# Optimization experiments

Measured on AMD Instinct MI355X. Metric: run time of the kernel, lower is better.

The kernel has to match this reference:

```python
import jax, jax.numpy as jnp
import numpy as np

N, A, C = 1024, 4096, 10000

def setup_inputs() -> dict:
    key = jax.random.key(0)
    ks = jax.random.split(key, 7)
    features = jax.random.normal(ks[0], (N, A), dtype=jnp.float32)
    labels = jax.random.randint(ks[1], (N,), 0, C, dtype=jnp.int64)
    fc_weight = jax.random.normal(ks[2], (C, A), dtype=jnp.float32) * 0.02
    fc_bias = jax.random.normal(ks[3], (C,), dtype=jnp.float32) * 0.02
    Ave = jax.random.normal(ks[4], (C, A), dtype=jnp.float32)
    CoVariance = jax.random.uniform(ks[5], (C, A), dtype=jnp.float32)
    Amount = jax.random.uniform(ks[6], (C,), dtype=jnp.float32) * 10.0
    return {"features": features, "labels": labels, "fc_weight": fc_weight,
            "fc_bias": fc_bias, "Ave": Ave, "CoVariance": CoVariance,
            "Amount": Amount, "ratio": 1}

def _update_cv(f, labels, Ave, CoVariance, Amount):
    # segment-reduce form of the onehot-masked mean/var in update_CV
    count = jax.ops.segment_sum(jnp.ones((f.shape[0],), f.dtype), labels, num_segments=C)  # [C]
    denom = jnp.maximum(count, 1.0)[:, None]                                               # [C,1]
    ave = jax.ops.segment_sum(f, labels, num_segments=C) / denom                           # [C,A]
    var = jax.ops.segment_sum((f - ave[labels]) ** 2, labels, num_segments=C) / denom      # [C,A]
    tot = count + Amount
    w = (count / jnp.where(tot == 0, 1.0, tot))[:, None]  # weight_CV, NaN->0 handled since count==0 when tot==0
    new_CV = CoVariance * (1.0 - w) + var * w + w * (1.0 - w) * (Ave - ave) ** 2
    new_Ave = Ave * (1.0 - w) + ave * w
    new_Amount = Amount + count
    return new_CV, new_Ave, new_Amount

def reference(features, labels, fc_weight, fc_bias, Ave, CoVariance, Amount, ratio):
    y = features @ fc_weight.T + fc_bias  # [N,C]
    f = jax.lax.stop_gradient(features)
    new_CV, new_Ave, new_Amount = _update_cv(f, labels, Ave, CoVariance, Amount)
    cv = jax.lax.stop_gradient(new_CV)
    # isda_aug: sigma2[n,c] = ratio * sum_a (W[c,a]-W[y_n,a])^2 * CV[y_n,a]
    # expanded into three GEMM/reduction terms to avoid the O(N*C*A) intermediate
    CVn = cv[labels]        # [N,A]
    Wk = fc_weight[labels]  # [N,A]
    term1 = CVn @ (fc_weight ** 2).T                          # [N,C]
    term2 = -2.0 * ((CVn * Wk) @ fc_weight.T)                 # [N,C]
    term3 = jnp.sum(CVn * Wk ** 2, axis=1, keepdims=True)     # [N,1]
    sigma2 = ratio * (term1 + term2 + term3)
    aug = y + 0.5 * sigma2
    logp = jax.nn.log_softmax(aug, axis=-1)
    loss = -jnp.mean(jnp.take_along_axis(logp, labels[:, None], axis=1))
    return (loss, y)
```

## Files before the change

kernel.cpp:

```cpp
#include <hip/hip_runtime.h>
#include <hip/hip_bf16.h>
#include <math.h>

#define NN 1024
#define AA 4096
#define CC 10000
#define NT 79
#define BM 64
#define BN 128

typedef __attribute__((ext_vector_type(8))) short short8;
typedef __attribute__((ext_vector_type(4))) float f32x4;

#define OFF_COUNT   0u
#define OFF_HEAD    40960u
#define OFF_NEXT    81920u
#define OFF_T3H     86016u
#define OFF_RAUG    90112u
#define OFF_PART    94208u
#define OFF_FEATB   741376u
#define OFF_A1B     9129984u
#define OFF_A2B     17518592u
#define WS_BASE     25907200u
#define OFF_WB      25907200u
#define WS_BIG      107827200u

#define A1OFF 8388608u
#define A2OFF 16777216u

__device__ inline unsigned short f2bf(float x) {
    union { float f; unsigned u; } v; v.f = x;
    unsigned r = v.u + 0x7FFFu + ((v.u >> 16) & 1u);
    return (unsigned short)(r >> 16);
}

__device__ __forceinline__ void gload16(const void* g, void* l) {
    __builtin_amdgcn_global_load_lds((const __attribute__((address_space(1))) void*)g,
                                     (__attribute__((address_space(3))) void*)l, 16, 0, 0);
}

__device__ __forceinline__ short8 bfsq(short8 w) {
    union U { short8 s; unsigned u[4]; } in, out;
    in.s = w;
    #pragma unroll
    for (int i = 0; i < 4; i++) {
        unsigned u = in.u[i];
        float lo = __uint_as_float(u << 16);
        float hi = __uint_as_float(u & 0xffff0000u);
        float sl = lo * lo;
        float sh = hi * hi;
        unsigned p;
        asm("v_cvt_pk_bf16_f32 %0, %1, %2" : "=v"(p) : "v"(sl), "v"(sh));
        out.u[i] = p;
    }
    return out.s;
}

__global__ void k_wconv(const float* __restrict__ fcw, unsigned short* __restrict__ wb) {
    const size_t total = (size_t)CC * AA / 4;
    for (size_t i = (size_t)blockIdx.x * 256 + threadIdx.x; i < total; i += (size_t)gridDim.x * 256) {
        float4 v = ((const float4*)fcw)[i];
        ushort4 b;
        b.x = f2bf(v.x); b.y = f2bf(v.y); b.z = f2bf(v.z); b.w = f2bf(v.w);
        ((ushort4*)wb)[i] = b;
    }
}

__global__ void k_count(const int* __restrict__ labels, int* count, int* head, int* nextp) {
    int n = blockIdx.x * 256 + threadIdx.x;
    if (n < NN) {
        int c = labels[n];
        atomicAdd(&count[c], 1);
        nextp[n] = atomicExch(&head[c], n);
    }
}

__global__ void k_rowprep(const float* __restrict__ feat, const int* __restrict__ labels,
                          const float* __restrict__ fcw, const float* __restrict__ Ave,
                          const float* __restrict__ CoV, const float* __restrict__ Amount,
                          const int* __restrict__ ratio_p, const int* __restrict__ count,
                          const int* __restrict__ head, const int* __restrict__ nextp,
                          unsigned short* __restrict__ featb, unsigned short* __restrict__ a1b,
                          unsigned short* __restrict__ a2b, float* __restrict__ t3h) {
    int n = blockIdx.x;
    int tid = threadIdx.x;
    int c = labels[n];
    float cnt = (float)count[c];
    float inv = 1.0f / cnt;
    float amt = Amount[c];
    float w = cnt / (cnt + amt);
    float omw = 1.0f - w;
    float w1w = w * omw;
    float rf = (float)(*ratio_p);
    const int h = head[c];
    float t3 = 0.f;
    #pragma unroll 1
    for (int i = 0; i < 4; i++) {
        int i4 = i * 256 + tid;
        float sf[4] = {0.f, 0.f, 0.f, 0.f};
        float sq[4] = {0.f, 0.f, 0.f, 0.f};
        float fvv[4] = {0.f, 0.f, 0.f, 0.f};
        for (int m = h; m >= 0; m = nextp[m]) {
            float4 v = ((const float4*)(feat + (size_t)m * AA))[i4];
            sf[0] += v.x; sf[1] += v.y; sf[2] += v.z; sf[3] += v.w;
            sq[0] += v.x * v.x; sq[1] += v.y * v.y;
            sq[2] += v.z * v.z; sq[3] += v.w * v.w;
            if (m == n) { fvv[0] = v.x; fvv[1] = v.y; fvv[2] = v.z; fvv[3] = v.w; }
        }
        float4 cov = ((const float4*)(CoV + (size_t)c * AA))[i4];
        float4 avv = ((const float4*)(Ave + (size_t)c * AA))[i4];
        float4 wkv = ((const float4*)(fcw + (size_t)c * AA))[i4];
        float cva[4] = {cov.x, cov.y, cov.z, cov.w};
        float ava[4] = {avv.x, avv.y, avv.z, avv.w};
        float wka[4] = {wkv.x, wkv.y, wkv.z, wkv.w};
        ushort4 fb, a1, a2;
        unsigned short ob[12];
        #pragma unroll
        for (int j = 0; j < 4; j++) {
            float ave = sf[j] * inv;
            float var = sq[j] * inv - ave * ave;
            float d = ava[j] - ave;
            float cv = cva[j] * omw + var * w + w1w * d * d;
            float wk = wka[j];
            ob[j]     = f2bf(fvv[j]);
            ob[4 + j] = f2bf(0.5f * rf * cv);
            ob[8 + j] = f2bf(-rf * cv * wk);
            t3 += 0.5f * rf * cv * wk * wk;
        }
        fb.x = ob[0]; fb.y = ob[1]; fb.z = ob[2]; fb.w = ob[3];
        a1.x = ob[4]; a1.y = ob[5]; a1.z = ob[6]; a1.w = ob[7];
        a2.x = ob[8]; a2.y = ob[9]; a2.z = ob[10]; a2.w = ob[11];
        size_t o = (size_t)n * AA + (size_t)i4 * 4;
        *(ushort4*)(featb + o) = fb;
        *(ushort4*)(a1b + o) = a1;
        *(ushort4*)(a2b + o) = a2;
    }
    #pragma unroll
    for (int m = 32; m >= 1; m >>= 1) t3 += __shfl_xor(t3, m, 64);
    __shared__ float red[4];
    if ((tid & 63) == 0) red[tid >> 6] = t3;
    __syncthreads();
    if (tid == 0) t3h[n] = red[0] + red[1] + red[2] + red[3];
}

__global__ __launch_bounds__(256, 4) void k_gemm(
    const unsigned short* __restrict__ featb, const unsigned short* __restrict__ wbp,
    const float* __restrict__ bias, const int* __restrict__ labels,
    const float* __restrict__ t3h, float* __restrict__ yout,
    float* __restrict__ rowaug, float* __restrict__ part) {
    __shared__ unsigned short sF[BM * 64];
    __shared__ unsigned short sA1[BM * 64];
    __shared__ unsigned short sA2[BM * 64];
    __shared__ unsigned short sW[BN * 64];

    const int tid = threadIdx.x;
    const int lane = tid & 63;
    const int wid = tid >> 6;
    const int lr = lane & 15, lk = lane >> 4;

    const int bid = blockIdx.x;
    const int wg = (bid & 7) * 158 + (bid >> 3);
    const int nb = wg >> 4;
    const int mb = wg & 15;
    const int brow = mb * BM, bcol = nb * BN;

    f32x4 accY[4][2], accS[4][2];
    f32x4 z = {0.f, 0.f, 0.f, 0.f};
    #pragma unroll
    for (int i = 0; i < 4; i++)
        #pragma unroll
        for (int j = 0; j < 2; j++) { accY[i][j] = z; accS[i][j] = z; }

    const int lrow8 = lane >> 3;
    const int cb = ((lane & 7) * 16) ^ (lrow8 << 4);
    const unsigned rowstep = 8u * AA * 2u;
    const unsigned abase = (unsigned)(brow + wid * 16 + lrow8) * (AA * 2u) + cb;
    const char* gA = (const char*)featb;
    unsigned woff[4];
    #pragma unroll
    for (int q = 0; q < 4; q++) {
        int cls = bcol + wid * 32 + q * 8 + lrow8;
        if (cls > CC - 1) cls = CC - 1;
        woff[q] = (unsigned)cls * (AA * 2u) + cb;
    }
    const int ldbA = wid * 2048;
    const int ldbW = wid * 4096;

    for (int kt = 0; kt < AA; kt += 64) {
        const unsigned ko = (unsigned)kt * 2u;
        #pragma unroll
        for (int q = 0; q < 2; q++) {
            const unsigned ao = abase + q * rowstep + ko;
            const int ld = ldbA + q * 1024;
            gload16(gA + ao, (char*)sF + ld);
            gload16(gA + A1OFF + ao, (char*)sA1 + ld);
            gload16(gA + A2OFF + ao, (char*)sA2 + ld);
        }
        #pragma unroll
        for (int q = 0; q < 4; q++) {
            gload16((const char*)wbp + (woff[q] + ko), (char*)sW + ldbW + q * 1024);
        }
        __syncthreads();
        #pragma unroll
        for (int k2 = 0; k2 < 2; k2++) {
            int kb = k2 * 64 + lk * 16;
            short8 bw[2], bw2[2];
            #pragma unroll
            for (int ni = 0; ni < 2; ni++) {
                int row = wid * 32 + ni * 16 + lr;
                int off = row * 128 + (kb ^ ((row & 7) << 4));
                bw[ni] = *(const short8*)((const char*)sW + off);
                bw2[ni] = bfsq(bw[ni]);
            }
            #pragma unroll
            for (int mi = 0; mi < 4; mi++) {
                int row = mi * 16 + lr;
                int off = row * 128 + (kb ^ ((row & 7) << 4));
                short8 af  = *(const short8*)((const char*)sF + off);
                short8 a1f = *(const short8*)((const char*)sA1 + off);
                short8 a2f = *(const short8*)((const char*)sA2 + off);
                #pragma unroll
                for (int ni = 0; ni < 2; ni++) {
                    accY[mi][ni] = __builtin_amdgcn_mfma_f32_16x16x32_bf16(af,  bw[ni],  accY[mi][ni], 0, 0, 0);
                    accS[mi][ni] = __builtin_amdgcn_mfma_f32_16x16x32_bf16(a1f, bw2[ni], accS[mi][ni], 0, 0, 0);
                    accS[mi][ni] = __builtin_amdgcn_mfma_f32_16x16x32_bf16(a2f, bw[ni],  accS[mi][ni], 0, 0, 0);
                }
            }
        }
        __syncthreads();
    }

    float* sRed = (float*)sF;
    #pragma unroll
    for (int mi = 0; mi < 4; mi++) {
        #pragma unroll
        for (int r = 0; r < 4; r++) {
            int rowt = mi * 16 + lk * 4 + r;
            int grow = brow + rowt;
            int lab = labels[grow];
            float t3 = t3h[grow];
            float av[2];
            #pragma unroll
            for (int ni = 0; ni < 2; ni++) {
                int gcol = bcol + wid * 32 + ni * 16 + lr;
                float acy = accY[mi][ni][r];
                if (gcol < CC) {
                    float yy = acy + bias[gcol];
                    yout[(size_t)grow * CC + gcol] = yy;
                    float aug = yy + accS[mi][ni][r] + t3;
                    if (gcol == lab) rowaug[grow] = aug;
                    av[ni] = aug;
                } else {
                    av[ni] = -3.0e38f;
                }
            }
            float ml = fmaxf(av[0], av[1]);
            #pragma unroll
            for (int m = 1; m < 16; m <<= 1) ml = fmaxf(ml, __shfl_xor(ml, m, 64));
            float sl = __expf(av[0] - ml) + __expf(av[1] - ml);
            #pragma unroll
            for (int m = 1; m < 16; m <<= 1) sl += __shfl_xor(sl, m, 64);
            if (lr == 0) {
                sRed[rowt * 8 + wid * 2 + 0] = ml;
                sRed[rowt * 8 + wid * 2 + 1] = sl;
            }
        }
    }
    __syncthreads();
    if (tid < 64) {
        float M = sRed[tid * 8 + 0];
        #pragma unroll
        for (int q = 1; q < 4; q++) M = fmaxf(M, sRed[tid * 8 + q * 2]);
        float S = 0.f;
        #pragma unroll
        for (int q = 0; q < 4; q++)
            S += sRed[tid * 8 + q * 2 + 1] * __expf(sRed[tid * 8 + q * 2] - M);
        size_t o = ((size_t)nb * NN + (brow + tid)) * 2;
        part[o] = M;
        part[o + 1] = S;
    }
}

__global__ __launch_bounds__(256, 2) void k_gemm_fb(
    const unsigned short* __restrict__ featb, const unsigned short* __restrict__ a1b,
    const unsigned short* __restrict__ a2b, const float* __restrict__ fcw,
    const float* __restrict__ bias, const int* __restrict__ labels,
    const float* __restrict__ t3h, float* __restrict__ yout,
    float* __restrict__ rowaug, float* __restrict__ part) {
    __shared__ unsigned short sF[128 * 64];
    __shared__ unsigned short sA1[128 * 64];
    __shared__ unsigned short sA2[128 * 64];
    __shared__ unsigned short sW[128 * 64];
    __shared__ unsigned short sW2[128 * 64];

    const int tid = threadIdx.x;
    const int lane = tid & 63;
    const int wid = tid >> 6;
    const int wr = wid >> 1, wc = wid & 1;
    const int lr = lane & 15, lk = lane >> 4;
    const int nb = blockIdx.x, mb = blockIdx.y;
    const int brow = mb * 128, bcol = nb * 128;

    f32x4 accY[4][4], accS[4][4];
    f32x4 z = {0.f, 0.f, 0.f, 0.f};
    #pragma unroll
    for (int i = 0; i < 4; i++)
        #pragma unroll
        for (int j = 0; j < 4; j++) { accY[i][j] = z; accS[i][j] = z; }

    const int srow = tid >> 3;
    const int sblk = tid & 7;

    for (int kt = 0; kt < AA; kt += 64) {
        #pragma unroll
        for (int p = 0; p < 4; p++) {
            int row = p * 32 + srow;
            size_t g = (size_t)(brow + row) * AA + kt + sblk * 8;
            int pos = row * 128 + ((sblk * 16) ^ ((row & 7) << 4));
            *(uint4*)((char*)sF + pos)  = *(const uint4*)(featb + g);
            *(uint4*)((char*)sA1 + pos) = *(const uint4*)(a1b + g);
            *(uint4*)((char*)sA2 + pos) = *(const uint4*)(a2b + g);
        }
        #pragma unroll
        for (int p = 0; p < 8; p++) {
            int idx = p * 256 + tid;
            int wrow = idx >> 4;
            int col4 = idx & 15;
            int cls = bcol + wrow;
            float4 wv = {0.f, 0.f, 0.f, 0.f};
            if (cls < CC) wv = *(const float4*)(fcw + (size_t)cls * AA + kt + col4 * 4);
            ushort4 wb, w2b;
            wb.x = f2bf(wv.x); wb.y = f2bf(wv.y); wb.z = f2bf(wv.z); wb.w = f2bf(wv.w);
            w2b.x = f2bf(wv.x * wv.x); w2b.y = f2bf(wv.y * wv.y);
            w2b.z = f2bf(wv.z * wv.z); w2b.w = f2bf(wv.w * wv.w);
            int pos = wrow * 128 + ((col4 * 8) ^ ((wrow & 7) << 4));
            *(ushort4*)((char*)sW + pos) = wb;
            *(ushort4*)((char*)sW2 + pos) = w2b;
        }
        __syncthreads();
        #pragma unroll
        for (int k2 = 0; k2 < 2; k2++) {
            int kb = k2 * 64 + lk * 16;
            short8 bw[4], bw2[4];
            #pragma unroll
            for (int ni = 0; ni < 4; ni++) {
                int row = wc * 64 + ni * 16 + lr;
                int off = row * 128 + (kb ^ ((row & 7) << 4));
                bw[ni]  = *(const short8*)((const char*)sW + off);
                bw2[ni] = *(const short8*)((const char*)sW2 + off);
            }
            #pragma unroll
            for (int mi = 0; mi < 4; mi++) {
                int row = wr * 64 + mi * 16 + lr;
                int off = row * 128 + (kb ^ ((row & 7) << 4));
                short8 af  = *(const short8*)((const char*)sF + off);
                short8 a1f = *(const short8*)((const char*)sA1 + off);
                short8 a2f = *(const short8*)((const char*)sA2 + off);
                #pragma unroll
                for (int ni = 0; ni < 4; ni++) {
                    accY[mi][ni] = __builtin_amdgcn_mfma_f32_16x16x32_bf16(af,  bw[ni],  accY[mi][ni], 0, 0, 0);
                    accS[mi][ni] = __builtin_amdgcn_mfma_f32_16x16x32_bf16(a1f, bw2[ni], accS[mi][ni], 0, 0, 0);
                    accS[mi][ni] = __builtin_amdgcn_mfma_f32_16x16x32_bf16(a2f, bw[ni],  accS[mi][ni], 0, 0, 0);
                }
            }
        }
        __syncthreads();
    }

    float* sRed = (float*)sF;
    #pragma unroll
    for (int mi = 0; mi < 4; mi++) {
        #pragma unroll
        for (int r = 0; r < 4; r++) {
            int rowt = wr * 64 + mi * 16 + lk * 4 + r;
            int grow = brow + rowt;
            int lab = labels[grow];
            float t3 = t3h[grow];
            float av[4];
            #pragma unroll
            for (int ni = 0; ni < 4; ni++) {
                int gcol = bcol + wc * 64 + ni * 16 + lr;
                float acy = accY[mi][ni][r];
                if (gcol < CC) {
                    float yy = acy + bias[gcol];
                    yout[(size_t)grow * CC + gcol] = yy;
                    float aug = yy + accS[mi][ni][r] + t3;
                    if (gcol == lab) rowaug[grow] = aug;
                    av[ni] = aug;
                } else {
                    av[ni] = -3.0e38f;
                }
            }
            float ml = fmaxf(fmaxf(av[0], av[1]), fmaxf(av[2], av[3]));
            #pragma unroll
            for (int m = 1; m < 16; m <<= 1) ml = fmaxf(ml, __shfl_xor(ml, m, 64));
            float sl = __expf(av[0] - ml) + __expf(av[1] - ml) +
                       __expf(av[2] - ml) + __expf(av[3] - ml);
            #pragma unroll
            for (int m = 1; m < 16; m <<= 1) sl += __shfl_xor(sl, m, 64);
            if (lr == 0) {
                sRed[rowt * 4 + wc * 2 + 0] = ml;
                sRed[rowt * 4 + wc * 2 + 1] = sl;
            }
        }
    }
    __syncthreads();
    if (tid < 128) {
        float m0 = sRed[tid * 4 + 0], s0 = sRed[tid * 4 + 1];
        float m1 = sRed[tid * 4 + 2], s1 = sRed[tid * 4 + 3];
        float M = fmaxf(m0, m1);
        float S = s0 * __expf(m0 - M) + s1 * __expf(m1 - M);
        size_t o = ((size_t)nb * NN + (brow + tid)) * 2;
        part[o] = M;
        part[o + 1] = S;
    }
}

__global__ void k_loss(const float* __restrict__ part, const float* __restrict__ rowaug,
                       float* __restrict__ out0) {
    __shared__ float red[256];
    int n = blockIdx.x * 256 + threadIdx.x;
    float M = -3.0e38f;
    for (int t = 0; t < NT; t++) M = fmaxf(M, part[((size_t)t * NN + n) * 2]);
    float S = 0.f;
    for (int t = 0; t < NT; t++) {
        float m = part[((size_t)t * NN + n) * 2];
        float s = part[((size_t)t * NN + n) * 2 + 1];
        S += s * __expf(m - M);
    }
    float lse = M + logf(S);
    float rl = lse - rowaug[n];
    red[threadIdx.x] = rl;
    __syncthreads();
    for (int st = 128; st > 0; st >>= 1) {
        if (threadIdx.x < st) red[threadIdx.x] += red[threadIdx.x + st];
        __syncthreads();
    }
    if (threadIdx.x == 0) atomicAdd(out0, red[0] * (1.0f / (float)NN));
}

extern "C" void kernel_launch(void* const* d_in, const int* in_sizes, int n_in,
                              void* d_out, int out_size, void* d_ws, size_t ws_size,
                              hipStream_t stream) {
    const float* feat   = (const float*)d_in[0];
    const int*   labels = (const int*)d_in[1];
    const float* fcw    = (const float*)d_in[2];
    const float* bias   = (const float*)d_in[3];
    const float* Ave    = (const float*)d_in[4];
    const float* CoV    = (const float*)d_in[5];
    const float* Amount = (const float*)d_in[6];
    const int*   ratio  = (const int*)d_in[7];

    if (ws_size < WS_BASE) return;
    const bool big = ws_size >= WS_BIG;

    char* w = (char*)d_ws;
    int*   count  = (int*)(w + OFF_COUNT);
    int*   head   = (int*)(w + OFF_HEAD);
    int*   nextp  = (int*)(w + OFF_NEXT);
    float* t3h    = (float*)(w + OFF_T3H);
    float* rowaug = (float*)(w + OFF_RAUG);
    float* part   = (float*)(w + OFF_PART);
    unsigned short* featb = (unsigned short*)(w + OFF_FEATB);
    unsigned short* a1b   = (unsigned short*)(w + OFF_A1B);
    unsigned short* a2b   = (unsigned short*)(w + OFF_A2B);
    unsigned short* wb    = (unsigned short*)(w + OFF_WB);

    float* out = (float*)d_out;
    float* yout = out + 1;

    hipMemsetAsync(w + OFF_COUNT, 0, 40960, stream);
    hipMemsetAsync(w + OFF_HEAD, 0xFF, 40960, stream);
    hipMemsetAsync(d_out, 0, 4, stream);

    if (big) k_wconv<<<dim3(2048), dim3(256), 0, stream>>>(fcw, wb);
    k_count<<<dim3(4), dim3(256), 0, stream>>>(labels, count, head, nextp);
    k_rowprep<<<dim3(NN), dim3(256), 0, stream>>>(feat, labels, fcw, Ave, CoV, Amount,
                                                  ratio, count, head, nextp,
                                                  featb, a1b, a2b, t3h);
    if (big) {
        k_gemm<<<dim3(16 * NT), dim3(256), 0, stream>>>(featb, wb, bias, labels,
                                                        t3h, yout, rowaug, part);
    } else {
        k_gemm_fb<<<dim3(NT, 8), dim3(256), 0, stream>>>(featb, a1b, a2b, fcw, bias, labels,
                                                         t3h, yout, rowaug, part);
    }
    k_loss<<<dim3(4), dim3(256), 0, stream>>>(part, rowaug, out);
}
```

Baseline: 358.4 us.

## Process two M-tiles per GEMM block with prefetch of next K-stage

Each GEMM workgroup now handles two 64-row tiles that share the same weight columns, so the grid shrinks to half. The loads for the next K step, or for the first step of the second tile, are issued after the compute barrier so they overlap the following iteration. Per-wave softmax partials are written straight to global memory, which drops the shared-memory cross-wave reduction, and k_loss now reduces four times as many partials. The workspace is enlarged to hold them. The risks are fewer blocks to fill the CUs and more partial traffic in k_loss.

```diff
diff --git a/kernel.cpp b/kernel.cpp
--- a/kernel.cpp
+++ b/kernel.cpp
@@ -18,12 +18,12 @@
 #define OFF_T3H     86016u
 #define OFF_RAUG    90112u
 #define OFF_PART    94208u
-#define OFF_FEATB   741376u
-#define OFF_A1B     9129984u
-#define OFF_A2B     17518592u
-#define WS_BASE     25907200u
-#define OFF_WB      25907200u
-#define WS_BIG      107827200u
+#define OFF_FEATB   2682880u
+#define OFF_A1B     11071488u
+#define OFF_A2B     19460096u
+#define WS_BASE     27848704u
+#define OFF_WB      27848704u
+#define WS_BIG      109768704u
 
 #define A1OFF 8388608u
 #define A2OFF 16777216u
@@ -159,22 +159,14 @@
     const int lr = lane & 15, lk = lane >> 4;
 
     const int bid = blockIdx.x;
-    const int wg = (bid & 7) * 158 + (bid >> 3);
-    const int nb = wg >> 4;
-    const int mb = wg & 15;
-    const int brow = mb * BM, bcol = nb * BN;
-
-    f32x4 accY[4][2], accS[4][2];
-    f32x4 z = {0.f, 0.f, 0.f, 0.f};
-    #pragma unroll
-    for (int i = 0; i < 4; i++)
-        #pragma unroll
-        for (int j = 0; j < 2; j++) { accY[i][j] = z; accS[i][j] = z; }
+    const int wg = (bid & 7) * 79 + (bid >> 3);
+    const int nb = wg >> 3;
+    const int mpair = wg & 7;
+    const int bcol = nb * BN;
 
     const int lrow8 = lane >> 3;
     const int cb = ((lane & 7) * 16) ^ (lrow8 << 4);
     const unsigned rowstep = 8u * AA * 2u;
-    const unsigned abase = (unsigned)(brow + wid * 16 + lrow8) * (AA * 2u) + cb;
     const char* gA = (const char*)featb;
     unsigned woff[4];
     #pragma unroll
@@ -185,100 +177,111 @@
     }
     const int ldbA = wid * 2048;
     const int ldbW = wid * 4096;
-
-    for (int kt = 0; kt < AA; kt += 64) {
-        const unsigned ko = (unsigned)kt * 2u;
-        #pragma unroll
-        for (int q = 0; q < 2; q++) {
-            const unsigned ao = abase + q * rowstep + ko;
-            const int ld = ldbA + q * 1024;
-            gload16(gA + ao, (char*)sF + ld);
-            gload16(gA + A1OFF + ao, (char*)sA1 + ld);
-            gload16(gA + A2OFF + ao, (char*)sA2 + ld);
-        }
-        #pragma unroll
-        for (int q = 0; q < 4; q++) {
-            gload16((const char*)wbp + (woff[q] + ko), (char*)sW + ldbW + q * 1024);
-        }
-        __syncthreads();
-        #pragma unroll
-        for (int k2 = 0; k2 < 2; k2++) {
-            int kb = k2 * 64 + lk * 16;
-            short8 bw[2], bw2[2];
-            #pragma unroll
-            for (int ni = 0; ni < 2; ni++) {
-                int row = wid * 32 + ni * 16 + lr;
-                int off = row * 128 + (kb ^ ((row & 7) << 4));
-                bw[ni] = *(const short8*)((const char*)sW + off);
-                bw2[ni] = bfsq(bw[ni]);
-            }
-            #pragma unroll
-            for (int mi = 0; mi < 4; mi++) {
-                int row = mi * 16 + lr;
-                int off = row * 128 + (kb ^ ((row & 7) << 4));
-                short8 af  = *(const short8*)((const char*)sF + off);
-                short8 a1f = *(const short8*)((const char*)sA1 + off);
-                short8 a2f = *(const short8*)((const char*)sA2 + off);
+    const unsigned abase0 = (unsigned)(mpair * 64 + wid * 16 + lrow8) * (AA * 2u) + cb;
+    const unsigned TILE2 = 512u * AA * 2u;
+
+#define STAGE(ab_, ko_) do {                                                 \
+    gload16(gA + (ab_) + (ko_), (char*)sF + ldbA);                           \
+    gload16(gA + (ab_) + rowstep + (ko_), (char*)sF + ldbA + 1024);          \
+    gload16(gA + A1OFF + (ab_) + (ko_), (char*)sA1 + ldbA);                  \
+    gload16(gA + A1OFF + (ab_) + rowstep + (ko_), (char*)sA1 + ldbA + 1024); \
+    gload16(gA + A2OFF + (ab_) + (ko_), (char*)sA2 + ldbA);                  \
+    gload16(gA + A2OFF + (ab_) + rowstep + (ko_), (char*)sA2 + ldbA + 1024); \
+    gload16((const char*)wbp + (woff[0] + (ko_)), (char*)sW + ldbW);         \
+    gload16((const char*)wbp + (woff[1] + (ko_)), (char*)sW + ldbW + 1024);  \
+    gload16((const char*)wbp + (woff[2] + (ko_)), (char*)sW + ldbW + 2048);  \
+    gload16((const char*)wbp + (woff[3] + (ko_)), (char*)sW + ldbW + 3072);  \
+} while (0)
+
+    STAGE(abase0, 0u);
+
+    #pragma unroll 1
+    for (int tt = 0; tt < 2; tt++) {
+        const unsigned ab = abase0 + (tt ? TILE2 : 0u);
+        const int brow = (mpair + 8 * tt) * 64;
+
+        f32x4 accY[4][2], accS[4][2];
+        f32x4 z = {0.f, 0.f, 0.f, 0.f};
+        #pragma unroll
+        for (int i = 0; i < 4; i++)
+            #pragma unroll
+            for (int j = 0; j < 2; j++) { accY[i][j] = z; accS[i][j] = z; }
+
+        #pragma unroll 1
+        for (int kt = 0; kt < AA; kt += 64) {
+            __syncthreads();
+            #pragma unroll
+            for (int k2 = 0; k2 < 2; k2++) {
+                int kb = k2 * 64 + lk * 16;
+                short8 bw[2], bw2[2];
                 #pragma unroll
                 for (int ni = 0; ni < 2; ni++) {
-                    accY[mi][ni] = __builtin_amdgcn_mfma_f32_16x16x32_bf16(af,  bw[ni],  accY[mi][ni], 0, 0, 0);
-                    accS[mi][ni] = __builtin_amdgcn_mfma_f32_16x16x32_bf16(a1f, bw2[ni], accS[mi][ni], 0, 0, 0);
-                    accS[mi][ni] = __builtin_amdgcn_mfma_f32_16x16x32_bf16(a2f, bw[ni],  accS[mi][ni], 0, 0, 0);
-                }
-            }
-        }
-        __syncthreads();
-    }
-
-    float* sRed = (float*)sF;
-    #pragma unroll
-    for (int mi = 0; mi < 4; mi++) {
-        #pragma unroll
-        for (int r = 0; r < 4; r++) {
-            int rowt = mi * 16 + lk * 4 + r;
-            int grow = brow + rowt;
-            int lab = labels[grow];
-            float t3 = t3h[grow];
-            float av[2];
-            #pragma unroll
-            for (int ni = 0; ni < 2; ni++) {
-                int gcol = bcol + wid * 32 + ni * 16 + lr;
-                float acy = accY[mi][ni][r];
-                if (gcol < CC) {
-                    float yy = acy + bias[gcol];
-                    yout[(size_t)grow * CC + gcol] = yy;
-                    float aug = yy + accS[mi][ni][r] + t3;
-                    if (gcol == lab) rowaug[grow] = aug;
-                    av[ni] = aug;
-                } else {
-                    av[ni] = -3.0e38f;
-                }
-            }
-            float ml = fmaxf(av[0], av[1]);
-            #pragma unroll
-            for (int m = 1; m < 16; m <<= 1) ml = fmaxf(ml, __shfl_xor(ml, m, 64));
-            float sl = __expf(av[0] - ml) + __expf(av[1] - ml);
-            #pragma unroll
-            for (int m = 1; m < 16; m <<= 1) sl += __shfl_xor(sl, m, 64);
-            if (lr == 0) {
-                sRed[rowt * 8 + wid * 2 + 0] = ml;
-                sRed[rowt * 8 + wid * 2 + 1] = sl;
-            }
-        }
-    }
-    __syncthreads();
-    if (tid < 64) {
-        float M = sRed[tid * 8 + 0];
-        #pragma unroll
-        for (int q = 1; q < 4; q++) M = fmaxf(M, sRed[tid * 8 + q * 2]);
-        float S = 0.f;
-        #pragma unroll
-        for (int q = 0; q < 4; q++)
-            S += sRed[tid * 8 + q * 2 + 1] * __expf(sRed[tid * 8 + q * 2] - M);
-        size_t o = ((size_t)nb * NN + (brow + tid)) * 2;
-        part[o] = M;
-        part[o + 1] = S;
-    }
+                    int row = wid * 32 + ni * 16 + lr;
+                    int off = row * 128 + (kb ^ ((row & 7) << 4));
+                    bw[ni] = *(const short8*)((const char*)sW + off);
+                    bw2[ni] = bfsq(bw[ni]);
+                }
+                #pragma unroll
+                for (int mi = 0; mi < 4; mi++) {
+                    int row = mi * 16 + lr;
+                    int off = row * 128 + (kb ^ ((row & 7) << 4));
+                    short8 af  = *(const short8*)((const char*)sF + off);
+                    short8 a1f = *(const short8*)((const char*)sA1 + off);
+                    short8 a2f = *(const short8*)((const char*)sA2 + off);
+                    #pragma unroll
+                    for (int ni = 0; ni < 2; ni++) {
+                        accY[mi][ni] = __builtin_amdgcn_mfma_f32_16x16x32_bf16(af,  bw[ni],  accY[mi][ni], 0, 0, 0);
+                        accS[mi][ni] = __builtin_amdgcn_mfma_f32_16x16x32_bf16(a1f, bw2[ni], accS[mi][ni], 0, 0, 0);
+                        accS[mi][ni] = __builtin_amdgcn_mfma_f32_16x16x32_bf16(a2f, bw[ni],  accS[mi][ni], 0, 0, 0);
+                    }
+                }
+            }
+            __syncthreads();
+            if (kt + 64 < AA) {
+                STAGE(ab, (unsigned)(kt + 64) * 2u);
+            } else if (tt == 0) {
+                STAGE(abase0 + TILE2, 0u);
+            }
+        }
+
+        #pragma unroll
+        for (int mi = 0; mi < 4; mi++) {
+            #pragma unroll
+            for (int r = 0; r < 4; r++) {
+                int rowt = mi * 16 + lk * 4 + r;
+                int grow = brow + rowt;
+                int lab = labels[grow];
+                float t3 = t3h[grow];
+                float av[2];
+                #pragma unroll
+                for (int ni = 0; ni < 2; ni++) {
+                    int gcol = bcol + wid * 32 + ni * 16 + lr;
+                    float acy = accY[mi][ni][r];
+                    if (gcol < CC) {
+                        float yy = acy + bias[gcol];
+                        yout[(size_t)grow * CC + gcol] = yy;
+                        float aug = yy + accS[mi][ni][r] + t3;
+                        if (gcol == lab) rowaug[grow] = aug;
+                        av[ni] = aug;
+                    } else {
+                        av[ni] = -3.0e38f;
+                    }
+                }
+                float ml = fmaxf(av[0], av[1]);
+                #pragma unroll
+                for (int m = 1; m < 16; m <<= 1) ml = fmaxf(ml, __shfl_xor(ml, m, 64));
+                float sl = __expf(av[0] - ml) + __expf(av[1] - ml);
+                #pragma unroll
+                for (int m = 1; m < 16; m <<= 1) sl += __shfl_xor(sl, m, 64);
+                if (lr == 0) {
+                    size_t p = ((size_t)(nb * 4 + wid) * NN + grow) * 2;
+                    part[p] = ml;
+                    part[p + 1] = sl;
+                }
+            }
+        }
+    }
+#undef STAGE
 }
 
 __global__ __launch_bounds__(256, 2) void k_gemm_fb(
@@ -417,13 +420,13 @@
 }
 
 __global__ void k_loss(const float* __restrict__ part, const float* __restrict__ rowaug,
-                       float* __restrict__ out0) {
+                       float* __restrict__ out0, int nparts) {
     __shared__ float red[256];
     int n = blockIdx.x * 256 + threadIdx.x;
     float M = -3.0e38f;
-    for (int t = 0; t < NT; t++) M = fmaxf(M, part[((size_t)t * NN + n) * 2]);
+    for (int t = 0; t < nparts; t++) M = fmaxf(M, part[((size_t)t * NN + n) * 2]);
     float S = 0.f;
-    for (int t = 0; t < NT; t++) {
+    for (int t = 0; t < nparts; t++) {
         float m = part[((size_t)t * NN + n) * 2];
         float s = part[((size_t)t * NN + n) * 2 + 1];
         S += s * __expf(m - M);
@@ -479,11 +482,12 @@
                                                   ratio, count, head, nextp,
                                                   featb, a1b, a2b, t3h);
     if (big) {
-        k_gemm<<<dim3(16 * NT), dim3(256), 0, stream>>>(featb, wb, bias, labels,
-                                                        t3h, yout, rowaug, part);
+        k_gemm<<<dim3(8 * NT), dim3(256), 0, stream>>>(featb, wb, bias, labels,
+                                                       t3h, yout, rowaug, part);
+        k_loss<<<dim3(4), dim3(256), 0, stream>>>(part, rowaug, out, NT * 4);
     } else {
         k_gemm_fb<<<dim3(NT, 8), dim3(256), 0, stream>>>(featb, a1b, a2b, fcw, bias, labels,
                                                          t3h, yout, rowaug, part);
-    }
-    k_loss<<<dim3(4), dim3(256), 0, stream>>>(part, rowaug, out);
-}
+        k_loss<<<dim3(4), dim3(256), 0, stream>>>(part, rowaug, out, NT);
+    }
+}
```

New measurement: 448.3 us. 25.1% more time.
